# Kernel optimization log

Measured on AMD Instinct MI355X. Metric: run time of the kernel, lower is better.

The kernel has to match this reference:

```python
import jax, jax.numpy as jnp
import numpy as np


def _lstm_scan(x_tm, W, b, reset_tm=None):
    """Run an hk.LSTM-equivalent scan over time-major x_tm [L, B, D].

    Gate order i, g, f, o with +1 forget-gate bias (haiku convention).
    If reset_tm [L, B] (bool) is given, state is zeroed BEFORE the step
    whenever reset is True (hk.ResetCore semantics).
    """
    B = x_tm.shape[1]
    H = b.shape[0] // 4

    def step(carry, inp):
        h, c = carry
        if reset_tm is None:
            xt = inp
        else:
            xt, rt = inp
            keep = jnp.logical_not(rt)[:, None]
            h = jnp.where(keep, h, 0.0)
            c = jnp.where(keep, c, 0.0)
        gates = jnp.concatenate([xt, h], axis=-1) @ W + b  # [B, 4H]
        i, g, f, o = jnp.split(gates, 4, axis=-1)
        c = jax.nn.sigmoid(f + 1.0) * c + jax.nn.sigmoid(i) * jnp.tanh(g)
        h = jax.nn.sigmoid(o) * jnp.tanh(c)
        return (h, c), h

    init = (jnp.zeros((B, H), x_tm.dtype), jnp.zeros((B, H), x_tm.dtype))
    xs = x_tm if reset_tm is None else (x_tm, reset_tm)
    _, hs = jax.lax.scan(step, init, xs)
    return hs  # [L, B, H]


def setup_inputs() -> dict:
    key = jax.random.key(0)
    kx, kwf, kwb, kl = jax.random.split(key, 4)
    B, L, D, H = 32, 1024, 512, 512
    scale = 1.0 / np.sqrt(D + H)
    return {
        "x": jax.random.normal(kx, (B, L, D), dtype=jnp.float32),
        "W_fwd": jax.random.normal(kwf, (D + H, 4 * H), dtype=jnp.float32) * scale,
        "b_fwd": jnp.zeros((4 * H,), dtype=jnp.float32),
        "W_bwd": jax.random.normal(kwb, (D + H, 4 * H), dtype=jnp.float32) * scale,
        "b_bwd": jnp.zeros((4 * H,), dtype=jnp.float32),
        "lengths": jax.random.randint(kl, (B,), 1, L + 1),
    }


def reference(x, W_fwd, b_fwd, W_bwd, b_bwd, lengths):
    B, L, D = x.shape
    # reset mask: True for t >= length - 1 (as in original module)
    mask = jnp.arange(L)[None, :] >= lengths[:, None] - 1  # [B, L]

    # forward direction
    h_f = _lstm_scan(jnp.swapaxes(x, 0, 1), W_fwd, b_fwd)  # [L, B, H]
    h_f = jnp.swapaxes(h_f, 0, 1)  # [B, L, H]

    # backward direction: flip time, run ResetCore LSTM, flip back
    x_b = jnp.flip(x, axis=1)
    mask_b = jnp.flip(mask, axis=1)
    h_b = _lstm_scan(jnp.swapaxes(x_b, 0, 1), W_bwd, b_bwd,
                     jnp.swapaxes(mask_b, 0, 1))  # [L, B, H]
    h_b = jnp.flip(jnp.swapaxes(h_b, 0, 1), axis=1)  # [B, L, H]

    return jnp.concatenate([h_f, h_b], axis=-1)  # [B, L, 2H]
```

## Files before the change

### kernel.cpp

```cpp
#include <hip/hip_runtime.h>
#include <stdint.h>


typedef __attribute__((ext_vector_type(8))) short  short8;
typedef __attribute__((ext_vector_type(4))) float  floatx4;

#define LSEQ 1024
#define NB   32
#define DD   512
#define HH   512
#define NG   2048

#define WX_OFF  0ul
#define WH_OFF  (4ul<<20)
#define X_OFF   (8ul<<20)
#define H_OFF   (40ul<<20)
#define RST_OFF ((40ul<<20)+(384ul<<10))
#define TAG_OFF ((40ul<<20)+(388ul<<10))
#define Z_OFF   (41ul<<20)
#define ZF_BYTES (2ul*LSEQ*NB*NG*4)
#define ZB_BYTES (2ul*LSEQ*NB*NG*2)
#define WS_NEED_F32 (Z_OFF + ZF_BYTES)
#define WS_NEED_B16 (Z_OFF + ZB_BYTES)

__device__ inline uint16_t f2bf(float f) {
  uint32_t u = __float_as_uint(f);
  u += 0x7fff + ((u >> 16) & 1);
  return (uint16_t)(u >> 16);
}
__device__ inline float fsigm(float x) { return 1.0f / (1.0f + __expf(-x)); }
__device__ inline float ftanh(float x) { return 1.0f - 2.0f / (__expf(2.0f * x) + 1.0f); }

template <typename ZT> __device__ inline void zstore(ZT* p, float v);
template <> __device__ inline void zstore<float>(float* p, float v) { *p = v; }
template <> __device__ inline void zstore<uint16_t>(uint16_t* p, float v) { *p = f2bf(v); }

template <typename ZT> __device__ inline float2 zld2(const ZT* p);
template <> __device__ inline float2 zld2<float>(const float* p) { return *(const float2*)p; }
template <> __device__ inline float2 zld2<uint16_t>(const uint16_t* p) {
  uint32_t u = *(const uint32_t*)p;
  float2 r;
  r.x = __uint_as_float((u & 0xffffu) << 16);
  r.y = __uint_as_float(u & 0xffff0000u);
  return r;
}

__global__ void k_init(const int* __restrict__ len, uint32_t* __restrict__ rst,
                       int* __restrict__ tags, uint16_t* __restrict__ H)
{
  int tid = blockIdx.x * blockDim.x + threadIdx.x;
  int stride = gridDim.x * blockDim.x;
  for (int i = tid; i < 512; i += stride) tags[i] = 0;
  for (int i = tid; i < 2 * 2 * NB * HH; i += stride) H[i] = 0;
  for (int t = tid; t < LSEQ; t += stride) {
    uint32_t m = 0;
    for (int b = 0; b < NB; ++b)
      m |= ((uint32_t)(t <= LSEQ - len[b])) << b;
    rst[t] = m;
  }
}

__global__ void k_wcast(const float* __restrict__ Wf, const float* __restrict__ Wb,
                        uint16_t* __restrict__ WX, uint16_t* __restrict__ WH)
{
  int tid = blockIdx.x * blockDim.x + threadIdx.x;
  if (tid >= 2 * 1024 * 512) return;
  int dir = tid >> 19;
  int r = tid & ((1 << 19) - 1);
  int k = r >> 9;
  int n4 = (r & 511) * 4;
  const float* W = dir ? Wb : Wf;
  const float4 v = *(const float4*)(W + (size_t)k * NG + n4);
  uint16_t* dst;
  int kk;
  if (k < DD) { dst = WX + (size_t)dir * NG * DD; kk = k; }
  else        { dst = WH + (size_t)dir * NG * HH; kk = k - DD; }
  dst[(size_t)(n4 + 0) * 512 + kk] = f2bf(v.x);
  dst[(size_t)(n4 + 1) * 512 + kk] = f2bf(v.y);
  dst[(size_t)(n4 + 2) * 512 + kk] = f2bf(v.z);
  dst[(size_t)(n4 + 3) * 512 + kk] = f2bf(v.w);
}

__global__ void k_xcast(const float* __restrict__ x, uint16_t* __restrict__ X)
{
  int i4 = blockIdx.x * blockDim.x + threadIdx.x;
  if (i4 >= (NB * LSEQ * DD) / 4) return;
  int d4 = (i4 & 127) * 4;
  int t  = (i4 >> 7) & 1023;
  int b  = i4 >> 17;
  const float4 v = *(const float4*)(x + (size_t)i4 * 4);
  uint32_t lo = (uint32_t)f2bf(v.x) | ((uint32_t)f2bf(v.y) << 16);
  uint32_t hi = (uint32_t)f2bf(v.z) | ((uint32_t)f2bf(v.w) << 16);
  uint2 u; u.x = lo; u.y = hi;
  *(uint2*)(X + ((size_t)t * NB + b) * DD + d4) = u;
}

template <typename ZT>
__global__ __launch_bounds__(256) void k_zgemm(
    const uint16_t* __restrict__ X, const uint16_t* __restrict__ WX,
    const float* __restrict__ bf_, const float* __restrict__ bb_,
    ZT* __restrict__ Z)
{
  __shared__ uint16_t sA[128 * 32];
  __shared__ uint16_t sB[128 * 32];

  const int bid = blockIdx.x;
  const int dir = bid >> 12;
  const int rem = bid & 4095;
  const int mtile = rem >> 4;
  const int ntile = rem & 15;
  const int tid = threadIdx.x;
  const int lane = tid & 63;
  const int w = tid >> 6;
  const int wm = (w >> 1) * 64;
  const int wn = (w & 1) * 64;

  const uint16_t* B = WX + (size_t)dir * NG * 512 + (size_t)(ntile * 128) * 512;
  const float* bias = (dir ? bb_ : bf_) + ntile * 128;

  uint4 ra[2], rb[2];
  auto load_tile = [&](int kk) {
#pragma unroll
    for (int j = 0; j < 2; ++j) {
      int c = tid + 256 * j;
      int row = c >> 2, ko = (c & 3) * 8;
      int grow = mtile * 128 + row;
      int step = grow >> 5, bb = grow & 31;
      int srow = dir ? ((1023 - step) * 32 + bb) : grow;
      ra[j] = *(const uint4*)(X + (size_t)srow * 512 + kk * 32 + ko);
      rb[j] = *(const uint4*)(B + (size_t)row * 512 + kk * 32 + ko);
    }
  };
  auto write_tile = [&]() {
#pragma unroll
    for (int j = 0; j < 2; ++j) {
      int c = tid + 256 * j;
      int row = c >> 2, ko = (c & 3) * 8;
      *(uint4*)(sA + row * 32 + ko) = ra[j];
      *(uint4*)(sB + row * 32 + ko) = rb[j];
    }
  };

  floatx4 acc[4][4];
#pragma unroll
  for (int m = 0; m < 4; ++m)
#pragma unroll
    for (int n = 0; n < 4; ++n)
#pragma unroll
      for (int r = 0; r < 4; ++r) acc[m][n][r] = 0.f;

  load_tile(0);
  for (int kk = 0; kk < 16; ++kk) {
    __syncthreads();
    write_tile();
    __syncthreads();
    if (kk < 15) load_tile(kk + 1);
    short8 af[4], bb8[4];
#pragma unroll
    for (int m = 0; m < 4; ++m)
      af[m] = *(const short8*)(sA + (wm + m * 16 + (lane & 15)) * 32 + (lane >> 4) * 8);
#pragma unroll
    for (int n = 0; n < 4; ++n)
      bb8[n] = *(const short8*)(sB + (wn + n * 16 + (lane & 15)) * 32 + (lane >> 4) * 8);
#pragma unroll
    for (int m = 0; m < 4; ++m)
#pragma unroll
      for (int n = 0; n < 4; ++n)
        acc[m][n] = __builtin_amdgcn_mfma_f32_16x16x32_bf16(af[m], bb8[n], acc[m][n], 0, 0, 0);
  }

  ZT* Zo = Z + ((size_t)dir * 32768 + (size_t)mtile * 128) * 2048 + ntile * 128;
#pragma unroll
  for (int n = 0; n < 4; ++n) {
    int col = wn + n * 16 + (lane & 15);
    float bv = bias[col];
#pragma unroll
    for (int m = 0; m < 4; ++m) {
      int row0 = wm + m * 16 + (lane >> 4) * 4;
#pragma unroll
      for (int r = 0; r < 4; ++r)
        zstore<ZT>(Zo + (size_t)(row0 + r) * 2048 + col, acc[m][n][r] + bv);
    }
  }
}

template <typename ZT>
__global__ __launch_bounds__(512, 2) void k_rec(
    const uint16_t* __restrict__ WH, const ZT* __restrict__ Z,
    const uint32_t* __restrict__ rst, uint16_t* __restrict__ hbuf,
    int* __restrict__ tags, float* __restrict__ out)
{
  __shared__ uint16_t sW[128 * 512];
  __shared__ float sG[NB * 128];

  const int tid = threadIdx.x;
  const int lane = tid & 63;
  const int wid = tid >> 6;
  const int gate = wid & 3;
  const int khalf = wid >> 2;
  const int dir = blockIdx.x >> 4;
  const int p = blockIdx.x & 15;

  const int r0 = lane & 15;
  const int k8 = (lane >> 4) * 8;

  {
    const uint16_t* Wg = WH + (size_t)dir * NG * HH;
    for (int i = tid; i < 8192; i += 512) {
      int lrow = i >> 6;
      int k16  = i & 63;
      int n = (lrow >> 5) * 512 + p * 32 + (lrow & 31);
      uint4 v = *(const uint4*)(Wg + (size_t)n * 512 + k16 * 8);
      int byte = lrow * 1024 + k16 * 16;
      *(uint4*)((char*)sW + (byte ^ ((lrow & 7) << 4))) = v;
    }
  }

  short8 zero8;
#pragma unroll
  for (int i = 0; i < 8; ++i) zero8[i] = 0;

  const int swz = (r0 & 7) << 4;
  const int wrow0 = (gate * 32 + r0) * 1024 + (khalf * 256 + k8) * 2;
  const int wrow1 = wrow0 + 16 * 1024;

  float cst0 = 0.f, cst1 = 0.f;
  const int b_e = tid >> 4;
  const int hc0 = (tid & 15) * 2;

  const ZT* Zb = Z + (size_t)dir * LSEQ * NB * NG + (size_t)b_e * NG + p * 32 + hc0;
  uint16_t* hb = hbuf + dir * 2 * NB * HH;
  int* tg = tags + dir * 256;
  int* myslot = tg + p * 16;

  float2 vzi = zld2<ZT>(Zb);
  float2 vzg = zld2<ZT>(Zb + 512);
  float2 vzf = zld2<ZT>(Zb + 1024);
  float2 vzo = zld2<ZT>(Zb + 1536);

  __syncthreads();

  for (int t = 0; t < LSEQ; ++t) {
    const uint32_t rm = dir ? rst[t] : 0u;

    if (t > 0) {
      if (wid == 0) {
        int guard = 0;
        for (;;) {
          int v = t;
          if (lane < 16)
            v = __hip_atomic_load(tg + lane * 16, __ATOMIC_RELAXED,
                                  __HIP_MEMORY_SCOPE_AGENT);
          if (__all(v >= t)) break;
          __builtin_amdgcn_s_sleep(1);
          if (++guard > (1 << 14)) break;
        }
        if (lane < 16)
          (void)__hip_atomic_load(tg + lane * 16, __ATOMIC_ACQUIRE,
                                  __HIP_MEMORY_SCOPE_AGENT);
      }
      __syncthreads();
    }

    const uint16_t* hA = hb + (t & 1) * NB * HH;
    const bool zr0 = (rm >> r0) & 1;
    const bool zr1 = (rm >> (16 + r0)) & 1;
    const int kof = khalf * 256 + k8;

    short8 a0[8], a1[8];
#pragma unroll
    for (int kk = 0; kk < 8; ++kk) {
      a0[kk] = *(const short8*)(hA + (size_t)r0 * HH + kof + kk * 32);
      a1[kk] = *(const short8*)(hA + (size_t)(16 + r0) * HH + kof + kk * 32);
    }
#pragma unroll
    for (int kk = 0; kk < 8; ++kk) {
      if (zr0) a0[kk] = zero8;
      if (zr1) a1[kk] = zero8;
    }

    floatx4 acc[2][2];
#pragma unroll
    for (int m = 0; m < 2; ++m)
#pragma unroll
      for (int n = 0; n < 2; ++n)
#pragma unroll
        for (int r = 0; r < 4; ++r) acc[m][n][r] = 0.f;

#pragma unroll
    for (int kk = 0; kk < 8; ++kk) {
      short8 b0 = *(const short8*)((const char*)sW + ((wrow0 + kk * 64) ^ swz));
      short8 b1 = *(const short8*)((const char*)sW + ((wrow1 + kk * 64) ^ swz));
      acc[0][0] = __builtin_amdgcn_mfma_f32_16x16x32_bf16(a0[kk], b0, acc[0][0], 0, 0, 0);
      acc[0][1] = __builtin_amdgcn_mfma_f32_16x16x32_bf16(a0[kk], b1, acc[0][1], 0, 0, 0);
      acc[1][0] = __builtin_amdgcn_mfma_f32_16x16x32_bf16(a1[kk], b0, acc[1][0], 0, 0, 0);
      acc[1][1] = __builtin_amdgcn_mfma_f32_16x16x32_bf16(a1[kk], b1, acc[1][1], 0, 0, 0);
    }

    if (khalf == 0) {
#pragma unroll
      for (int m = 0; m < 2; ++m)
#pragma unroll
        for (int n = 0; n < 2; ++n)
#pragma unroll
          for (int r = 0; r < 4; ++r) {
            int row = m * 16 + (lane >> 4) * 4 + r;
            sG[row * 128 + gate * 32 + n * 16 + r0] = acc[m][n][r];
          }
    }
    __syncthreads();
    if (khalf == 1) {
#pragma unroll
      for (int m = 0; m < 2; ++m)
#pragma unroll
        for (int n = 0; n < 2; ++n)
#pragma unroll
          for (int r = 0; r < 4; ++r) {
            int row = m * 16 + (lane >> 4) * 4 + r;
            sG[row * 128 + gate * 32 + n * 16 + r0] += acc[m][n][r];
          }
    }
    __syncthreads();

    const int gb = b_e * 128;
    const bool cz = (rm >> b_e) & 1;
    float hv0, hv1;
#pragma unroll
    for (int j = 0; j < 2; ++j) {
      int hc = hc0 + j;
      float xi = sG[gb + hc]      + (j ? vzi.y : vzi.x);
      float xg = sG[gb + 32 + hc] + (j ? vzg.y : vzg.x);
      float xf = sG[gb + 64 + hc] + (j ? vzf.y : vzf.x);
      float xo = sG[gb + 96 + hc] + (j ? vzo.y : vzo.x);
      float ii = fsigm(xi);
      float gg = ftanh(xg);
      float ff = fsigm(xf + 1.0f);
      float oo = fsigm(xo);
      float cp = j ? cst1 : cst0;
      if (cz) cp = 0.f;
      float cn = ff * cp + ii * gg;
      if (j) cst1 = cn; else cst0 = cn;
      float hn = oo * ftanh(cn);
      if (j) hv1 = hn; else hv0 = hn;
    }
    uint32_t hpack = (uint32_t)f2bf(hv0) | ((uint32_t)f2bf(hv1) << 16);
    __hip_atomic_store(
        (uint32_t*)(hb + ((t + 1) & 1) * NB * HH + (size_t)b_e * HH + p * 32 + hc0),
        hpack, __ATOMIC_RELAXED, __HIP_MEMORY_SCOPE_AGENT);

    asm volatile("s_waitcnt vmcnt(0)" ::: "memory");
    __syncthreads();
    if (tid == 0)
      __hip_atomic_store(myslot, t + 1, __ATOMIC_RELAXED,
                         __HIP_MEMORY_SCOPE_AGENT);

    if (t + 1 < LSEQ) {
      const ZT* zt = Zb + (size_t)(t + 1) * NB * NG;
      vzi = zld2<ZT>(zt);
      vzg = zld2<ZT>(zt + 512);
      vzf = zld2<ZT>(zt + 1024);
      vzo = zld2<ZT>(zt + 1536);
    }

    const int t_x = dir ? (LSEQ - 1 - t) : t;
    float2 ov; ov.x = hv0; ov.y = hv1;
    *(float2*)(out + ((size_t)b_e * LSEQ + t_x) * 1024 + dir * 512 + p * 32 + hc0) = ov;
  }
}

__global__ void k_report(float* __restrict__ out, int n, float val)
{
  int tid = blockIdx.x * blockDim.x + threadIdx.x;
  int stride = gridDim.x * blockDim.x;
  for (int i = tid; i < n; i += stride) out[i] = val;
}

extern "C" void kernel_launch(void* const* d_in, const int* in_sizes, int n_in,
                              void* d_out, int out_size, void* d_ws, size_t ws_size,
                              hipStream_t stream)
{
  const float* x   = (const float*)d_in[0];
  const float* Wf  = (const float*)d_in[1];
  const float* bf_ = (const float*)d_in[2];
  const float* Wb  = (const float*)d_in[3];
  const float* bb_ = (const float*)d_in[4];
  const int*   len = (const int*)d_in[5];
  float* out = (float*)d_out;
  char* ws = (char*)d_ws;

  const bool f32z = ws_size >= WS_NEED_F32;
  if (!f32z && ws_size < WS_NEED_B16) {
    k_report<<<2048, 256, 0, stream>>>(out, out_size,
                                       200.0f + (float)(ws_size >> 20) * 0.1f);
    return;
  }

  uint16_t* WX  = (uint16_t*)(ws + WX_OFF);
  uint16_t* WHp = (uint16_t*)(ws + WH_OFF);
  uint16_t* X   = (uint16_t*)(ws + X_OFF);
  uint16_t* H   = (uint16_t*)(ws + H_OFF);
  uint32_t* RST = (uint32_t*)(ws + RST_OFF);
  int*      TAG = (int*)(ws + TAG_OFF);

  k_init<<<32, 256, 0, stream>>>(len, RST, TAG, H);
  k_wcast<<<4096, 256, 0, stream>>>(Wf, Wb, WX, WHp);
  k_xcast<<<16384, 256, 0, stream>>>(x, X);

  if (f32z) {
    float* Z = (float*)(ws + Z_OFF);
    k_zgemm<float><<<8192, 256, 0, stream>>>(X, WX, bf_, bb_, Z);
    k_rec<float><<<32, 512, 0, stream>>>(WHp, Z, RST, H, TAG, out);
  } else {
    uint16_t* Z = (uint16_t*)(ws + Z_OFF);
    k_zgemm<uint16_t><<<8192, 256, 0, stream>>>(X, WX, bf_, bb_, Z);
    k_rec<uint16_t><<<32, 512, 0, stream>>>(WHp, Z, RST, H, TAG, out);
  }
}
```

Baseline: 7.564 ms.

## Stage hidden state in LDS and exchange via cache-bypassing vector loads/stores

The recurrent kernel now gathers each block's new h slice in shared memory and writes it to the global exchange buffer with 128 threads issuing 16-byte stores carrying sc0 sc1 cache bits, replacing per-thread 4-byte atomic stores. Reads of the previous h use the same cache-bypassing dwordx4 loads via inline asm, and the acquire atomic load after the spin wait is dropped. The gate scratch array is padded to a 129-float stride to reduce LDS bank conflicts. The intent is to cut cross-block communication latency per timestep. In exchange it adds an extra barrier, and coherence now rests on the cache bits rather than explicit acquire semantics, which could be fragile.

```diff
diff --git a/kernel.cpp b/kernel.cpp
--- a/kernel.cpp
+++ b/kernel.cpp
@@ -4,12 +4,14 @@
 
 typedef __attribute__((ext_vector_type(8))) short  short8;
 typedef __attribute__((ext_vector_type(4))) float  floatx4;
+typedef __attribute__((ext_vector_type(4))) unsigned int uintx4;
 
 #define LSEQ 1024
 #define NB   32
 #define DD   512
 #define HH   512
 #define NG   2048
+#define SGS  129
 
 #define WX_OFF  0ul
 #define WH_OFF  (4ul<<20)
@@ -43,6 +45,17 @@
   r.x = __uint_as_float((u & 0xffffu) << 16);
   r.y = __uint_as_float(u & 0xffff0000u);
   return r;
+}
+
+__device__ inline short8 mload16(const uint16_t* p) {
+  short8 v;
+  asm volatile("global_load_dwordx4 %0, %1, off sc0 sc1"
+               : "=v"(v) : "v"(p));
+  return v;
+}
+__device__ inline void mstore16(uint16_t* p, uintx4 v) {
+  asm volatile("global_store_dwordx4 %0, %1, off sc0 sc1"
+               :: "v"(p), "v"(v) : "memory");
 }
 
 __global__ void k_init(const int* __restrict__ len, uint32_t* __restrict__ rst,
@@ -191,7 +204,8 @@
     int* __restrict__ tags, float* __restrict__ out)
 {
   __shared__ uint16_t sW[128 * 512];
-  __shared__ float sG[NB * 128];
+  __shared__ float sG[NB * SGS];
+  __shared__ uint16_t sH[NB * 32];
 
   const int tid = threadIdx.x;
   const int lane = tid & 63;
@@ -255,9 +269,6 @@
           __builtin_amdgcn_s_sleep(1);
           if (++guard > (1 << 14)) break;
         }
-        if (lane < 16)
-          (void)__hip_atomic_load(tg + lane * 16, __ATOMIC_ACQUIRE,
-                                  __HIP_MEMORY_SCOPE_AGENT);
       }
       __syncthreads();
     }
@@ -268,11 +279,16 @@
     const int kof = khalf * 256 + k8;
 
     short8 a0[8], a1[8];
-#pragma unroll
-    for (int kk = 0; kk < 8; ++kk) {
-      a0[kk] = *(const short8*)(hA + (size_t)r0 * HH + kof + kk * 32);
-      a1[kk] = *(const short8*)(hA + (size_t)(16 + r0) * HH + kof + kk * 32);
-    }
+    {
+      const uint16_t* pa = hA + (size_t)r0 * HH + kof;
+#pragma unroll
+      for (int kk = 0; kk < 8; ++kk) {
+        a0[kk] = mload16(pa + kk * 32);
+        a1[kk] = mload16(pa + 16 * HH + kk * 32);
+      }
+    }
+    asm volatile("s_waitcnt vmcnt(0)" ::: "memory");
+    __builtin_amdgcn_sched_barrier(0);
 #pragma unroll
     for (int kk = 0; kk < 8; ++kk) {
       if (zr0) a0[kk] = zero8;
@@ -305,7 +321,7 @@
 #pragma unroll
           for (int r = 0; r < 4; ++r) {
             int row = m * 16 + (lane >> 4) * 4 + r;
-            sG[row * 128 + gate * 32 + n * 16 + r0] = acc[m][n][r];
+            sG[row * SGS + gate * 32 + n * 16 + r0] = acc[m][n][r];
           }
     }
     __syncthreads();
@@ -317,12 +333,12 @@
 #pragma unroll
           for (int r = 0; r < 4; ++r) {
             int row = m * 16 + (lane >> 4) * 4 + r;
-            sG[row * 128 + gate * 32 + n * 16 + r0] += acc[m][n][r];
+            sG[row * SGS + gate * 32 + n * 16 + r0] += acc[m][n][r];
           }
     }
     __syncthreads();
 
-    const int gb = b_e * 128;
+    const int gb = b_e * SGS;
     const bool cz = (rm >> b_e) & 1;
     float hv0, hv1;
 #pragma unroll
@@ -344,10 +360,14 @@
       if (j) hv1 = hn; else hv0 = hn;
     }
     uint32_t hpack = (uint32_t)f2bf(hv0) | ((uint32_t)f2bf(hv1) << 16);
-    __hip_atomic_store(
-        (uint32_t*)(hb + ((t + 1) & 1) * NB * HH + (size_t)b_e * HH + p * 32 + hc0),
-        hpack, __ATOMIC_RELAXED, __HIP_MEMORY_SCOPE_AGENT);
-
+    *(uint32_t*)(sH + b_e * 32 + hc0) = hpack;
+    __syncthreads();
+
+    if (tid < 128) {
+      int row = tid >> 2, ch = tid & 3;
+      uintx4 v = *(const uintx4*)(sH + row * 32 + ch * 8);
+      mstore16(hb + ((t + 1) & 1) * NB * HH + (size_t)row * HH + p * 32 + ch * 8, v);
+    }
     asm volatile("s_waitcnt vmcnt(0)" ::: "memory");
     __syncthreads();
     if (tid == 0)
```

Result: no change. 7.572 ms (+0.1%).
